# Performance work log

Measured on AMD Instinct MI355X. Metric: run time of the kernel, lower is better.

The kernel has to match this reference:

```python
import jax, jax.numpy as jnp
import numpy as np

ATTEN_DIM = 64

def setup_inputs() -> dict:
    key = jax.random.key(0)
    ks = jax.random.split(key, 7)
    b, c, h, w = 16, 2048, 32, 32
    d_att, d_emb = 64, 64
    x = jax.random.normal(ks[0], (b, c, h, w), dtype=jnp.float32)
    # 1x1 conv == per-position linear; store weights as [out, in]
    scale = 1.0 / np.sqrt(c)
    wq = jax.random.normal(ks[1], (d_att, c), dtype=jnp.float32) * scale
    wk = jax.random.normal(ks[2], (d_att, c), dtype=jnp.float32) * scale
    wv = jax.random.normal(ks[3], (d_emb, c), dtype=jnp.float32) * scale
    bq = jnp.zeros((d_att,), dtype=jnp.float32)
    bk = jnp.zeros((d_att,), dtype=jnp.float32)
    bv = jnp.zeros((d_emb,), dtype=jnp.float32)
    return {"x": x, "wq": wq, "bq": bq, "wk": wk, "bk": bk, "wv": wv, "bv": bv}


def reference(x, wq, bq, wk, bk, wv, bv):
    b, c, h, w = x.shape
    # 1x1 conv projections: [b,c,h,w] x [d,c] -> [b,d,h,w]
    q = jnp.einsum('bchw,dc->bdhw', x, wq) + bq[None, :, None, None]
    k = jnp.einsum('bchw,dc->bdhw', x, wk) + bk[None, :, None, None]
    v = jnp.einsum('bchw,dc->bdhw', x, wv) + bv[None, :, None, None]
    # full non-local attention scores [b, h, w, h, w]
    atten = jnp.einsum('bcxy,bcij->bxyij', q, k) / ATTEN_DIM  # NOTE: module divides by atten_dim, not sqrt
    atten = jax.nn.softmax(atten.reshape(b, h, w, h * w), axis=-1).reshape(b, h, w, h, w)
    out = jnp.einsum('bxyij,bdij->bxyd', atten, v)
    return jnp.transpose(out, (0, 3, 1, 2))  # [b, emb_dim, h, w]
```

## Files before the change

kernel.cpp:

```cpp
#include <hip/hip_runtime.h>

typedef float f32x4 __attribute__((ext_vector_type(4)));
typedef short s16x8 __attribute__((ext_vector_type(8)));
typedef unsigned short u16;
typedef unsigned short u16x8 __attribute__((ext_vector_type(8)));

__device__ __forceinline__ u16 f2bf(float f) {
  unsigned u = __builtin_bit_cast(unsigned, f);
  u += 0x7fffu + ((u >> 16) & 1u);
  return (u16)(u >> 16);
}

__device__ __forceinline__ unsigned cvt_pk_bf16(float a, float b) {
  unsigned r;
  asm("v_cvt_pk_bf16_f32 %0, %1, %2" : "=v"(r) : "v"(a), "v"(b));
  return r;
}

#define AS1 __attribute__((address_space(1)))
#define AS3 __attribute__((address_space(3)))
#define GLD16(g, l) __builtin_amdgcn_global_load_lds((const AS1 unsigned int*)(g), (AS3 unsigned int*)(l), 16, 0, 0)

__global__ __launch_bounds__(256) void prepack_w(
    const float* __restrict__ wq, const float* __restrict__ wk, const float* __restrict__ wv,
    u16* __restrict__ Wpk)
{
  const int d = blockIdx.x;
  const int t = threadIdx.x;
  const int kc = t >> 3, blk = t & 7;
  const int key = (d >> 1) & 7;
  const float* src = (d < 64) ? (wq + (size_t)d * 2048)
                   : (d < 128) ? (wk + (size_t)(d - 64) * 2048)
                               : (wv + (size_t)(d - 128) * 2048);
  const float* s8 = src + kc * 64 + ((blk ^ key) << 3);
  u16x8 o;
#pragma unroll
  for (int j = 0; j < 8; ++j) o[j] = f2bf(s8[j]);
  *(u16x8*)(Wpk + ((size_t)(kc * 192 + d) << 6) + (blk << 3)) = o;
}

__global__ __launch_bounds__(512) void qkv_proj(
    const float* __restrict__ x, const u16* __restrict__ Wpk,
    const float* __restrict__ bq, const float* __restrict__ bk, const float* __restrict__ bv,
    u16* __restrict__ Qo, u16* __restrict__ Ko, u16* __restrict__ Vt)
{
  const int b   = blockIdx.x >> 4;
  const int p0  = (blockIdx.x & 15) * 64;
  const int tid = threadIdx.x;
  const int lane = tid & 63;
  const int wid  = tid >> 6;
  const int l15 = lane & 15, l4 = lane >> 4;
  const int wm = wid & 1, wn = wid >> 1;

  __shared__ __align__(16) u16 lA[4][64 * 64];
  __shared__ __align__(16) u16 lB[4][192 * 64];

  const int pg = lane & 15;
  const int kb = wid * 4 + (lane >> 4);
  const int k0 = kb * 4;
  const int ww = wid - 4;

  f32x4 acc[2][3];
#pragma unroll
  for (int m = 0; m < 2; ++m)
#pragma unroll
    for (int n = 0; n < 3; ++n) acc[m][n] = (f32x4)(0.0f);

  const float* xb = x + (size_t)b * 2048 * 1024 + p0 + pg * 4;

  float4 SA[8], SB[8];

  auto xload2 = [&](int c, float4 (&S)[8]) {
#pragma unroll
    for (int cc = 0; cc < 2; ++cc) {
      const float* g = xb + (size_t)((c + cc) * 64 + k0) * 1024;
#pragma unroll
      for (int r = 0; r < 4; ++r) S[cc * 4 + r] = *(const float4*)(g + r * 1024);
    }
  };
  auto xstore2 = [&](int c, float4 (&S)[8]) {
#pragma unroll
    for (int cc = 0; cc < 2; ++cc) {
      const int slot = (c + cc) & 3;
#pragma unroll
      for (int col = 0; col < 4; ++col) {
        int p = pg * 4 + col;
        unsigned lo = cvt_pk_bf16(S[cc * 4 + 0][col], S[cc * 4 + 1][col]);
        unsigned hi = cvt_pk_bf16(S[cc * 4 + 2][col], S[cc * 4 + 3][col]);
        int swz = ((kb >> 1) ^ ((p >> 1) & 7)) & 7;
        char* dst = (char*)&lA[0][0] + slot * 8192 + p * 128 + (swz << 4) + (kb & 1) * 8;
        *(uint2*)dst = make_uint2(lo, hi);
      }
    }
  };
  auto wissue2 = [&](int c) {
#pragma unroll
    for (int cc = 0; cc < 2; ++cc) {
      const int slot = (c + cc) & 3;
      const u16* g = Wpk + (size_t)(c + cc) * 12288 + lane * 8;
#pragma unroll
      for (int j = 0; j < 6; ++j) {
        int q = ww * 6 + j;
        GLD16(g + q * 512, &lB[0][0] + slot * 12288 + q * 512);
      }
    }
  };
  auto domfma = [&](int slot) {
#pragma unroll
    for (int ks = 0; ks < 2; ++ks) {
      s16x8 af[2], bfv[3];
#pragma unroll
      for (int m = 0; m < 2; ++m) {
        int p = wm * 32 + m * 16 + l15;
        int swz = ((ks * 4 + l4) ^ ((p >> 1) & 7)) & 7;
        af[m] = *(const s16x8*)((const char*)&lA[0][0] + slot * 8192 + p * 128 + (swz << 4));
      }
#pragma unroll
      for (int n = 0; n < 3; ++n) {
        int d = wn * 48 + n * 16 + l15;
        int swz = ((ks * 4 + l4) ^ ((d >> 1) & 7)) & 7;
        bfv[n] = *(const s16x8*)((const char*)&lB[0][0] + slot * 24576 + d * 128 + (swz << 4));
      }
#pragma unroll
      for (int m = 0; m < 2; ++m)
#pragma unroll
        for (int n = 0; n < 3; ++n)
          acc[m][n] = __builtin_amdgcn_mfma_f32_16x16x32_bf16(af[m], bfv[n], acc[m][n], 0, 0, 0);
    }
  };
  auto barrier = [&]() {
    if (wid < 4) asm volatile("s_waitcnt lgkmcnt(0)" ::: "memory");
    else         asm volatile("s_waitcnt vmcnt(0) lgkmcnt(0)" ::: "memory");
    __builtin_amdgcn_sched_barrier(0);
    __builtin_amdgcn_s_barrier();
    __builtin_amdgcn_sched_barrier(0);
  };
  auto step = [&](int t, float4 (&Sl)[8], float4 (&Ss)[8]) {
    if (wid < 4) { if (t < 14) xload2(2 * t + 4, Sl); }
    else         { if (t < 15) wissue2(2 * t + 2); }
    __builtin_amdgcn_s_setprio(1);
    domfma((2 * t) & 3);
    domfma((2 * t + 1) & 3);
    __builtin_amdgcn_s_setprio(0);
    if (wid < 4 && t < 15) xstore2(2 * t + 2, Ss);
    barrier();
  };

  if (wid < 4) { xload2(0, SA); xload2(2, SB); xstore2(0, SA); }
  else         { wissue2(0); }
  barrier();

  for (int tt = 0; tt < 8; ++tt) {
    step(2 * tt,     SA, SB);
    step(2 * tt + 1, SB, SA);
  }

#pragma unroll
  for (int n = 0; n < 3; ++n) {
    const int dg = wn * 48 + n * 16 + l15;
    const int wi = dg >> 6, dl = dg & 63;
    const float* bsrc = (wi == 0) ? bq : (wi == 1) ? bk : bv;
    const float bias = bsrc[dl];
#pragma unroll
    for (int m = 0; m < 2; ++m) {
      const int pl = wm * 32 + m * 16 + l4 * 4;
      f32x4 a = acc[m][n];
      if (wi < 2) {
        u16* dst = (wi == 0 ? Qo : Ko) + ((size_t)b * 1024 + p0 + pl) * 64 + dl;
#pragma unroll
        for (int r = 0; r < 4; ++r) dst[(size_t)r * 64] = f2bf(a[r] + bias);
      } else {
        ushort4 hh;
        hh.x = f2bf(a[0] + bias); hh.y = f2bf(a[1] + bias);
        hh.z = f2bf(a[2] + bias); hh.w = f2bf(a[3] + bias);
        *(ushort4*)(Vt + ((size_t)b * 64 + dl) * 1024 + p0 + pl) = hh;
      }
    }
  }
}

__global__ __launch_bounds__(256) void attn_kernel(
    const u16* __restrict__ Qg, const u16* __restrict__ Kg,
    const u16* __restrict__ Vg, float* __restrict__ Po, float* __restrict__ lp)
{
  const int bid = blockIdx.x;
  const int b  = bid >> 5;
  const int qt = (bid >> 1) & 15;
  const int h  = bid & 1;
  const int q0 = qt * 64;
  const int tid = threadIdx.x;
  const int lane = tid & 63;
  const int wid = tid >> 6;
  const int l15 = lane & 15, l4 = lane >> 4;
  const int qb = q0 + wid * 16;

  __shared__ __align__(16) u16 lK[2][128 * 64];
  __shared__ __align__(16) u16 lV[2][64 * 128];
  __shared__ __align__(16) u16 lP[4][16 * 128];

  s16x8 qa[2];
#pragma unroll
  for (int ks = 0; ks < 2; ++ks)
    qa[ks] = *(const s16x8*)(Qg + ((size_t)b * 1024 + qb + l15) * 64 + ks * 32 + l4 * 8);

  float l_run[4];
  f32x4 oacc[4];
#pragma unroll
  for (int r = 0; r < 4; ++r) l_run[r] = 0.f;
#pragma unroll
  for (int n = 0; n < 4; ++n) oacc[n] = (f32x4)(0.0f);

  u16x8 kp[4], vp[4];
  auto load_kv = [&](int kc) {
    const int pk0 = kc * 128;
#pragma unroll
    for (int i = 0; i < 4; ++i) {
      int idx = tid + 256 * i;
      int row = idx >> 3, blk = idx & 7;
      kp[i] = *(const u16x8*)(Kg + ((size_t)b * 1024 + pk0 + row) * 64 + blk * 8);
      int vr = idx >> 4, vbk = idx & 15;
      vp[i] = *(const u16x8*)(Vg + ((size_t)b * 64 + vr) * 1024 + pk0 + vbk * 8);
    }
  };
  auto store_kv = [&](int buf) {
#pragma unroll
    for (int i = 0; i < 4; ++i) {
      int idx = tid + 256 * i;
      int row = idx >> 3, blk = idx & 7;
      *(u16x8*)(&lK[buf][0] + row * 64 + ((blk ^ ((row >> 1) & 7)) << 3)) = kp[i];
      int vr = idx >> 4, vbk = idx & 15;
      *(u16x8*)(&lV[buf][0] + vr * 128 + ((vbk ^ ((vr & 7) << 1)) << 3)) = vp[i];
    }
  };

  const int kc0 = h * 4;
  load_kv(kc0); store_kv(0); __syncthreads();

  const float CEXP = 0.0225422933f;

  for (int ic = 0; ic < 4; ++ic) {
    const int cur = ic & 1;
    if (ic + 1 < 4) load_kv(kc0 + ic + 1);

    f32x4 sacc[8];
#pragma unroll
    for (int n = 0; n < 8; ++n) sacc[n] = (f32x4)(0.0f);
#pragma unroll
    for (int ks = 0; ks < 2; ++ks) {
#pragma unroll
      for (int n = 0; n < 8; ++n) {
        int row = n * 16 + l15;
        s16x8 kv = *(const s16x8*)(&lK[cur][0] + row * 64 +
                     (((ks * 4 + l4) ^ ((row >> 1) & 7)) << 3));
        sacc[n] = __builtin_amdgcn_mfma_f32_16x16x32_bf16(qa[ks], kv, sacc[n], 0, 0, 0);
      }
    }

#pragma unroll
    for (int r = 0; r < 4; ++r) {
      const int prow = l4 * 4 + r;
      float psum = 0.f;
#pragma unroll
      for (int n = 0; n < 8; ++n) {
        float pv = exp2f(sacc[n][r] * CEXP);
        psum += pv;
        int blk = (n * 2 + (l15 >> 3)) ^ ((prow & 7) << 1);
        lP[wid][prow * 128 + blk * 8 + (l15 & 7)] = f2bf(pv);
      }
      psum += __shfl_xor(psum, 1);
      psum += __shfl_xor(psum, 2);
      psum += __shfl_xor(psum, 4);
      psum += __shfl_xor(psum, 8);
      l_run[r] += psum;
    }

#pragma unroll
    for (int ks = 0; ks < 4; ++ks) {
      s16x8 pfr = *(const s16x8*)(&lP[wid][0] + l15 * 128 +
                    (((ks * 4 + l4) ^ ((l15 & 7) << 1)) << 3));
#pragma unroll
      for (int n = 0; n < 4; ++n) {
        int row = n * 16 + l15;
        s16x8 vv = *(const s16x8*)(&lV[cur][0] + row * 128 +
                     (((ks * 4 + l4) ^ ((row & 7) << 1)) << 3));
        oacc[n] = __builtin_amdgcn_mfma_f32_16x16x32_bf16(pfr, vv, oacc[n], 0, 0, 0);
      }
    }

    if (ic + 1 < 4) store_kv(cur ^ 1);
    __syncthreads();
  }

#pragma unroll
  for (int n = 0; n < 4; ++n) {
    const int d = n * 16 + l15;
    float4 o;
    o.x = oacc[n][0]; o.y = oacc[n][1]; o.z = oacc[n][2]; o.w = oacc[n][3];
    *(float4*)(Po + (((size_t)h * 16 + b) * 64 + d) * 1024 + q0 + wid * 16 + l4 * 4) = o;
  }
  if (l15 == 0) {
#pragma unroll
    for (int r = 0; r < 4; ++r)
      lp[((size_t)h * 16 + b) * 1024 + qb + l4 * 4 + r] = l_run[r];
  }
}

__global__ __launch_bounds__(256) void attn_merge(
    const float* __restrict__ Po, const float* __restrict__ lp, float* __restrict__ out)
{
  const int i = (blockIdx.x * 256 + threadIdx.x) * 4;
  float4 a = *(const float4*)(Po + i);
  float4 c = *(const float4*)(Po + 1048576 + i);
  const int b = i >> 16;
  const int p = i & 1023;
  const float* l0 = lp + b * 1024 + p;
  const float* l1 = lp + 16384 + b * 1024 + p;
  float4 o;
  o.x = (a.x + c.x) / (l0[0] + l1[0]);
  o.y = (a.y + c.y) / (l0[1] + l1[1]);
  o.z = (a.z + c.z) / (l0[2] + l1[2]);
  o.w = (a.w + c.w) / (l0[3] + l1[3]);
  *(float4*)(out + i) = o;
}

extern "C" void kernel_launch(void* const* d_in, const int* in_sizes, int n_in,
                              void* d_out, int out_size, void* d_ws, size_t ws_size,
                              hipStream_t stream) {
  const float* x  = (const float*)d_in[0];
  const float* wq = (const float*)d_in[1];
  const float* bq = (const float*)d_in[2];
  const float* wk = (const float*)d_in[3];
  const float* bk = (const float*)d_in[4];
  const float* wv = (const float*)d_in[5];
  const float* bv = (const float*)d_in[6];
  float* out = (float*)d_out;

  u16* Qo  = (u16*)d_ws;
  u16* Ko  = Qo + (size_t)16 * 1024 * 64;
  u16* Vt  = Ko + (size_t)16 * 1024 * 64;
  u16* Wpk = Vt + (size_t)16 * 1024 * 64;
  float* Po = (float*)(Wpk + (size_t)32 * 192 * 64);
  float* lpart = Po + (size_t)2 * 16 * 64 * 1024;

  prepack_w<<<192, 256, 0, stream>>>(wq, wk, wv, Wpk);
  qkv_proj<<<256, 512, 0, stream>>>(x, Wpk, bq, bk, bv, Qo, Ko, Vt);
  attn_kernel<<<512, 256, 0, stream>>>(Qo, Ko, Vt, Po, lpart);
  attn_merge<<<1024, 256, 0, stream>>>(Po, lpart, out);
}
```

Baseline: 58.76 us.

## Restructure QKV projection into split-K wave groups with all-wave loading

The QKV projection kernel drops the producer/consumer wave split, where four waves loaded x and four loaded W. All eight waves now share the x and W loads with double-buffered LDS, and the two wave groups alternate on K-chunks. Each wave computes a full 64x48 tile, and the two groups' partial accumulators are reduced through LDS at the end. This aims to spread load latency across all waves and overlap it with MFMA, at the cost of a barrier every chunk, an extra LDS reduction, and more accumulator registers per wave.

```diff
diff --git a/kernel.cpp b/kernel.cpp
--- a/kernel.cpp
+++ b/kernel.cpp
@@ -50,130 +50,138 @@
   const int lane = tid & 63;
   const int wid  = tid >> 6;
   const int l15 = lane & 15, l4 = lane >> 4;
-  const int wm = wid & 1, wn = wid >> 1;
-
-  __shared__ __align__(16) u16 lA[4][64 * 64];
-  __shared__ __align__(16) u16 lB[4][192 * 64];
-
-  const int pg = lane & 15;
-  const int kb = wid * 4 + (lane >> 4);
-  const int k0 = kb * 4;
-  const int ww = wid - 4;
-
-  f32x4 acc[2][3];
-#pragma unroll
-  for (int m = 0; m < 2; ++m)
+  const int cw  = wid & 3;
+  const int grp = wid >> 2;
+
+  __shared__ __align__(16) char smem[65536];
+
+  const int kbq = wid * 2 + (l4 >> 1);
+  const int rp  = (l4 & 1) * 2;
+  const int pc0 = l15 * 4;
+
+  f32x4 acc[4][3];
+#pragma unroll
+  for (int m = 0; m < 4; ++m)
 #pragma unroll
     for (int n = 0; n < 3; ++n) acc[m][n] = (f32x4)(0.0f);
 
-  const float* xb = x + (size_t)b * 2048 * 1024 + p0 + pg * 4;
-
-  float4 SA[8], SB[8];
-
-  auto xload2 = [&](int c, float4 (&S)[8]) {
-#pragma unroll
-    for (int cc = 0; cc < 2; ++cc) {
-      const float* g = xb + (size_t)((c + cc) * 64 + k0) * 1024;
-#pragma unroll
-      for (int r = 0; r < 4; ++r) S[cc * 4 + r] = *(const float4*)(g + r * 1024);
-    }
-  };
-  auto xstore2 = [&](int c, float4 (&S)[8]) {
-#pragma unroll
-    for (int cc = 0; cc < 2; ++cc) {
-      const int slot = (c + cc) & 3;
-#pragma unroll
-      for (int col = 0; col < 4; ++col) {
-        int p = pg * 4 + col;
-        unsigned lo = cvt_pk_bf16(S[cc * 4 + 0][col], S[cc * 4 + 1][col]);
-        unsigned hi = cvt_pk_bf16(S[cc * 4 + 2][col], S[cc * 4 + 3][col]);
-        int swz = ((kb >> 1) ^ ((p >> 1) & 7)) & 7;
-        char* dst = (char*)&lA[0][0] + slot * 8192 + p * 128 + (swz << 4) + (kb & 1) * 8;
-        *(uint2*)dst = make_uint2(lo, hi);
-      }
-    }
-  };
-  auto wissue2 = [&](int c) {
-#pragma unroll
-    for (int cc = 0; cc < 2; ++cc) {
-      const int slot = (c + cc) & 3;
-      const u16* g = Wpk + (size_t)(c + cc) * 12288 + lane * 8;
-#pragma unroll
-      for (int j = 0; j < 6; ++j) {
-        int q = ww * 6 + j;
-        GLD16(g + q * 512, &lB[0][0] + slot * 12288 + q * 512);
-      }
+  const float* xb = x + (size_t)b * 2048 * 1024 + p0 + pc0;
+  float4 xr[2][2];
+
+  auto xissue = [&](int c, int buf) {
+    const float* g = xb + (size_t)(c * 64 + kbq * 4 + rp) * 1024;
+    xr[buf][0] = *(const float4*)g;
+    xr[buf][1] = *(const float4*)(g + 1024);
+  };
+  auto xwrite = [&](int c, int buf) {
+    char* base = smem + (c & 1) * 8192;
+#pragma unroll
+    for (int col = 0; col < 4; ++col) {
+      int p = pc0 + col;
+      unsigned pk = cvt_pk_bf16(xr[buf][0][col], xr[buf][1][col]);
+      char* dst = base + p * 128 + (((kbq >> 1) ^ ((p >> 1) & 7)) << 4)
+                + (kbq & 1) * 8 + (rp >> 1) * 4;
+      *(unsigned*)dst = pk;
+    }
+  };
+  auto wissue = [&](int c) {
+    const u16* g = Wpk + (size_t)c * 12288 + lane * 8;
+    char* base = smem + 16384 + (c & 1) * 24576;
+#pragma unroll
+    for (int j = 0; j < 3; ++j) {
+      int q = wid * 3 + j;
+      GLD16(g + q * 512, base + q * 1024);
     }
   };
   auto domfma = [&](int slot) {
+    const char* aB = smem + slot * 8192;
+    const char* bB = smem + 16384 + slot * 24576;
 #pragma unroll
     for (int ks = 0; ks < 2; ++ks) {
-      s16x8 af[2], bfv[3];
-#pragma unroll
-      for (int m = 0; m < 2; ++m) {
-        int p = wm * 32 + m * 16 + l15;
+      s16x8 af[4], bfv[3];
+#pragma unroll
+      for (int m = 0; m < 4; ++m) {
+        int p = m * 16 + l15;
         int swz = ((ks * 4 + l4) ^ ((p >> 1) & 7)) & 7;
-        af[m] = *(const s16x8*)((const char*)&lA[0][0] + slot * 8192 + p * 128 + (swz << 4));
+        af[m] = *(const s16x8*)(aB + p * 128 + (swz << 4));
       }
 #pragma unroll
       for (int n = 0; n < 3; ++n) {
-        int d = wn * 48 + n * 16 + l15;
+        int d = cw * 48 + n * 16 + l15;
         int swz = ((ks * 4 + l4) ^ ((d >> 1) & 7)) & 7;
-        bfv[n] = *(const s16x8*)((const char*)&lB[0][0] + slot * 24576 + d * 128 + (swz << 4));
-      }
-#pragma unroll
-      for (int m = 0; m < 2; ++m)
+        bfv[n] = *(const s16x8*)(bB + d * 128 + (swz << 4));
+      }
+#pragma unroll
+      for (int m = 0; m < 4; ++m)
 #pragma unroll
         for (int n = 0; n < 3; ++n)
           acc[m][n] = __builtin_amdgcn_mfma_f32_16x16x32_bf16(af[m], bfv[n], acc[m][n], 0, 0, 0);
     }
   };
-  auto barrier = [&]() {
-    if (wid < 4) asm volatile("s_waitcnt lgkmcnt(0)" ::: "memory");
-    else         asm volatile("s_waitcnt vmcnt(0) lgkmcnt(0)" ::: "memory");
+
+  wissue(0);
+  xissue(0, 0);
+  xissue(1, 1);
+  asm volatile("s_waitcnt vmcnt(2)" ::: "memory");
+  __builtin_amdgcn_sched_barrier(0);
+  xwrite(0, 0);
+  asm volatile("s_waitcnt lgkmcnt(0)" ::: "memory");
+  __builtin_amdgcn_sched_barrier(0);
+  __builtin_amdgcn_s_barrier();
+  __builtin_amdgcn_sched_barrier(0);
+
+  for (int c = 0; c < 32; ++c) {
+    if (c < 31) wissue(c + 1);
+    if (c < 30) xissue(c + 2, c & 1);
+    if (grp == (c & 1)) {
+      __builtin_amdgcn_s_setprio(1);
+      domfma(c & 1);
+      __builtin_amdgcn_s_setprio(0);
+    }
+    if (c < 31) xwrite(c + 1, (c + 1) & 1);
+    if (c < 30) asm volatile("s_waitcnt vmcnt(2) lgkmcnt(0)" ::: "memory");
+    else        asm volatile("s_waitcnt vmcnt(0) lgkmcnt(0)" ::: "memory");
     __builtin_amdgcn_sched_barrier(0);
     __builtin_amdgcn_s_barrier();
     __builtin_amdgcn_sched_barrier(0);
-  };
-  auto step = [&](int t, float4 (&Sl)[8], float4 (&Ss)[8]) {
-    if (wid < 4) { if (t < 14) xload2(2 * t + 4, Sl); }
-    else         { if (t < 15) wissue2(2 * t + 2); }
-    __builtin_amdgcn_s_setprio(1);
-    domfma((2 * t) & 3);
-    domfma((2 * t + 1) & 3);
-    __builtin_amdgcn_s_setprio(0);
-    if (wid < 4 && t < 15) xstore2(2 * t + 2, Ss);
-    barrier();
-  };
-
-  if (wid < 4) { xload2(0, SA); xload2(2, SB); xstore2(0, SA); }
-  else         { wissue2(0); }
-  barrier();
-
-  for (int tt = 0; tt < 8; ++tt) {
-    step(2 * tt,     SA, SB);
-    step(2 * tt + 1, SB, SA);
-  }
-
-#pragma unroll
-  for (int n = 0; n < 3; ++n) {
-    const int dg = wn * 48 + n * 16 + l15;
-    const int wi = dg >> 6, dl = dg & 63;
-    const float* bsrc = (wi == 0) ? bq : (wi == 1) ? bk : bv;
-    const float bias = bsrc[dl];
-#pragma unroll
-    for (int m = 0; m < 2; ++m) {
-      const int pl = wm * 32 + m * 16 + l4 * 4;
-      f32x4 a = acc[m][n];
-      if (wi < 2) {
-        u16* dst = (wi == 0 ? Qo : Ko) + ((size_t)b * 1024 + p0 + pl) * 64 + dl;
-#pragma unroll
-        for (int r = 0; r < 4; ++r) dst[(size_t)r * 64] = f2bf(a[r] + bias);
-      } else {
-        ushort4 hh;
-        hh.x = f2bf(a[0] + bias); hh.y = f2bf(a[1] + bias);
-        hh.z = f2bf(a[2] + bias); hh.w = f2bf(a[3] + bias);
-        *(ushort4*)(Vt + ((size_t)b * 64 + dl) * 1024 + p0 + pl) = hh;
+  }
+
+  if (grp == 1) {
+#pragma unroll
+    for (int m = 0; m < 4; ++m)
+#pragma unroll
+      for (int n = 0; n < 3; ++n)
+        *(f32x4*)(smem + cw * 12288 + ((m * 3 + n) * 64 + lane) * 16) = acc[m][n];
+  }
+  asm volatile("s_waitcnt lgkmcnt(0)" ::: "memory");
+  __builtin_amdgcn_s_barrier();
+  if (grp == 0) {
+#pragma unroll
+    for (int m = 0; m < 4; ++m)
+#pragma unroll
+      for (int n = 0; n < 3; ++n)
+        acc[m][n] += *(const f32x4*)(smem + cw * 12288 + ((m * 3 + n) * 64 + lane) * 16);
+
+#pragma unroll
+    for (int n = 0; n < 3; ++n) {
+      const int dg = cw * 48 + n * 16 + l15;
+      const int wi = dg >> 6, dl = dg & 63;
+      const float* bsrc = (wi == 0) ? bq : (wi == 1) ? bk : bv;
+      const float bias = bsrc[dl];
+#pragma unroll
+      for (int m = 0; m < 4; ++m) {
+        const int pl = m * 16 + l4 * 4;
+        f32x4 a = acc[m][n];
+        if (wi < 2) {
+          u16* dst = (wi == 0 ? Qo : Ko) + ((size_t)b * 1024 + p0 + pl) * 64 + dl;
+#pragma unroll
+          for (int r = 0; r < 4; ++r) dst[(size_t)r * 64] = f2bf(a[r] + bias);
+        } else {
+          ushort4 hh;
+          hh.x = f2bf(a[0] + bias); hh.y = f2bf(a[1] + bias);
+          hh.z = f2bf(a[2] + bias); hh.w = f2bf(a[3] + bias);
+          *(ushort4*)(Vt + ((size_t)b * 64 + dl) * 1024 + p0 + pl) = hh;
+        }
       }
     }
   }
```

Measured after the change: 80.43 us. 1.37x slower.

## Pre-swizzle K/V in projection and stream tiles via direct global-to-LDS loads

Applied to the files above, without the earlier changes.

The projection epilogue now folds the softmax exponent scale into Q and writes K and V already in the swizzled LDS layout. This lets the attention kernel use global_load_lds DMA to fill double-buffered K/V tiles with vmcnt-based waits instead of register staging. It also raises wave priority around the MFMA phases and packs P to bf16 in pairs. This removes register round-trips and the per-element scale multiply. The cost is tighter coupling between the producer's stored layout and the consumer's swizzle.

```diff
diff --git a/kernel.cpp b/kernel.cpp
--- a/kernel.cpp
+++ b/kernel.cpp
@@ -20,6 +20,8 @@
 #define AS1 __attribute__((address_space(1)))
 #define AS3 __attribute__((address_space(3)))
 #define GLD16(g, l) __builtin_amdgcn_global_load_lds((const AS1 unsigned int*)(g), (AS3 unsigned int*)(l), 16, 0, 0)
+
+#define CEXP 0.0225421101f
 
 __global__ __launch_bounds__(256) void prepack_w(
     const float* __restrict__ wq, const float* __restrict__ wk, const float* __restrict__ wv,
@@ -67,7 +69,6 @@
     for (int n = 0; n < 3; ++n) acc[m][n] = (f32x4)(0.0f);
 
   const float* xb = x + (size_t)b * 2048 * 1024 + p0 + pg * 4;
-
   float4 SA[8], SB[8];
 
   auto xload2 = [&](int c, float4 (&S)[8]) {
@@ -165,15 +166,25 @@
     for (int m = 0; m < 2; ++m) {
       const int pl = wm * 32 + m * 16 + l4 * 4;
       f32x4 a = acc[m][n];
-      if (wi < 2) {
-        u16* dst = (wi == 0 ? Qo : Ko) + ((size_t)b * 1024 + p0 + pl) * 64 + dl;
-#pragma unroll
-        for (int r = 0; r < 4; ++r) dst[(size_t)r * 64] = f2bf(a[r] + bias);
+      if (wi == 0) {
+        u16* dst = Qo + ((size_t)b * 1024 + p0 + pl) * 64 + dl;
+#pragma unroll
+        for (int r = 0; r < 4; ++r) dst[(size_t)r * 64] = f2bf((a[r] + bias) * CEXP);
+      } else if (wi == 1) {
+#pragma unroll
+        for (int r = 0; r < 4; ++r) {
+          const int p = p0 + pl + r;
+          Ko[((size_t)b * 1024 + p) * 64 + (((dl >> 3) ^ ((p >> 1) & 7)) << 3) + (dl & 7)]
+            = f2bf(a[r] + bias);
+        }
       } else {
+        const int pk0 = p0 + pl;
         ushort4 hh;
         hh.x = f2bf(a[0] + bias); hh.y = f2bf(a[1] + bias);
         hh.z = f2bf(a[2] + bias); hh.w = f2bf(a[3] + bias);
-        *(ushort4*)(Vt + ((size_t)b * 64 + dl) * 1024 + p0 + pl) = hh;
+        u16* dst = Vt + ((size_t)b * 64 + dl) * 1024 + (pk0 & ~127)
+                 + (((((pk0 >> 3) & 15) ^ ((dl & 7) << 1)) & 15) << 3) + (pk0 & 7);
+        *(ushort4*)dst = hh;
       }
     }
   }
@@ -190,9 +201,9 @@
   const int q0 = qt * 64;
   const int tid = threadIdx.x;
   const int lane = tid & 63;
-  const int wid = tid >> 6;
+  const int w = tid >> 6;
   const int l15 = lane & 15, l4 = lane >> 4;
-  const int qb = q0 + wid * 16;
+  const int qb = q0 + w * 16;
 
   __shared__ __align__(16) u16 lK[2][128 * 64];
   __shared__ __align__(16) u16 lV[2][64 * 128];
@@ -203,6 +214,9 @@
   for (int ks = 0; ks < 2; ++ks)
     qa[ks] = *(const s16x8*)(Qg + ((size_t)b * 1024 + qb + l15) * 64 + ks * 32 + l4 * 8);
 
+  const u16* Kb = Kg + (size_t)b * 65536;
+  const u16* Vb = Vg + (size_t)b * 65536;
+
   float l_run[4];
   f32x4 oacc[4];
 #pragma unroll
@@ -210,62 +224,50 @@
 #pragma unroll
   for (int n = 0; n < 4; ++n) oacc[n] = (f32x4)(0.0f);
 
-  u16x8 kp[4], vp[4];
-  auto load_kv = [&](int kc) {
-    const int pk0 = kc * 128;
-#pragma unroll
-    for (int i = 0; i < 4; ++i) {
-      int idx = tid + 256 * i;
-      int row = idx >> 3, blk = idx & 7;
-      kp[i] = *(const u16x8*)(Kg + ((size_t)b * 1024 + pk0 + row) * 64 + blk * 8);
-      int vr = idx >> 4, vbk = idx & 15;
-      vp[i] = *(const u16x8*)(Vg + ((size_t)b * 64 + vr) * 1024 + pk0 + vbk * 8);
-    }
-  };
-  auto store_kv = [&](int buf) {
-#pragma unroll
-    for (int i = 0; i < 4; ++i) {
-      int idx = tid + 256 * i;
-      int row = idx >> 3, blk = idx & 7;
-      *(u16x8*)(&lK[buf][0] + row * 64 + ((blk ^ ((row >> 1) & 7)) << 3)) = kp[i];
-      int vr = idx >> 4, vbk = idx & 15;
-      *(u16x8*)(&lV[buf][0] + vr * 128 + ((vbk ^ ((vr & 7) << 1)) << 3)) = vp[i];
-    }
-  };
-
-  const int kc0 = h * 4;
-  load_kv(kc0); store_kv(0); __syncthreads();
-
-  const float CEXP = 0.0225422933f;
-
-  for (int ic = 0; ic < 4; ++ic) {
-    const int cur = ic & 1;
-    if (ic + 1 < 4) load_kv(kc0 + ic + 1);
-
+  auto kv_issue = [&](int tile, int buf) {
+    const int pk0 = tile * 128;
+#pragma unroll
+    for (int jj = 0; jj < 4; ++jj)
+      GLD16(Kb + (size_t)(pk0 + w * 32 + jj * 8) * 64 + lane * 8,
+            (char*)&lK[buf][0] + (w * 4 + jj) * 1024);
+#pragma unroll
+    for (int jj = 0; jj < 4; ++jj)
+      GLD16(Vb + (size_t)(w * 16 + jj * 4 + (lane >> 4)) * 1024 + pk0 + (lane & 15) * 8,
+            (char*)&lV[buf][0] + (w * 4 + jj) * 1024);
+  };
+
+  auto compute = [&](int buf) {
     f32x4 sacc[8];
 #pragma unroll
     for (int n = 0; n < 8; ++n) sacc[n] = (f32x4)(0.0f);
+    __builtin_amdgcn_s_setprio(1);
 #pragma unroll
     for (int ks = 0; ks < 2; ++ks) {
 #pragma unroll
       for (int n = 0; n < 8; ++n) {
         int row = n * 16 + l15;
-        s16x8 kv = *(const s16x8*)(&lK[cur][0] + row * 64 +
+        s16x8 kv = *(const s16x8*)(&lK[buf][0] + row * 64 +
                      (((ks * 4 + l4) ^ ((row >> 1) & 7)) << 3));
         sacc[n] = __builtin_amdgcn_mfma_f32_16x16x32_bf16(qa[ks], kv, sacc[n], 0, 0, 0);
       }
     }
+    __builtin_amdgcn_s_setprio(0);
 
 #pragma unroll
     for (int r = 0; r < 4; ++r) {
       const int prow = l4 * 4 + r;
+      const int key = (prow & 7) << 1;
+      float pv[8];
       float psum = 0.f;
 #pragma unroll
-      for (int n = 0; n < 8; ++n) {
-        float pv = exp2f(sacc[n][r] * CEXP);
-        psum += pv;
-        int blk = (n * 2 + (l15 >> 3)) ^ ((prow & 7) << 1);
-        lP[wid][prow * 128 + blk * 8 + (l15 & 7)] = f2bf(pv);
+      for (int n = 0; n < 8; ++n) { pv[n] = exp2f(sacc[n][r]); psum += pv[n]; }
+#pragma unroll
+      for (int n = 0; n < 8; n += 2) {
+        unsigned pk = cvt_pk_bf16(pv[n], pv[n + 1]);
+        int blk0 = (n * 2 + (l15 >> 3)) ^ key;
+        int blk1 = ((n + 1) * 2 + (l15 >> 3)) ^ key;
+        lP[w][prow * 128 + blk0 * 8 + (l15 & 7)] = (u16)pk;
+        lP[w][prow * 128 + blk1 * 8 + (l15 & 7)] = (u16)(pk >> 16);
       }
       psum += __shfl_xor(psum, 1);
       psum += __shfl_xor(psum, 2);
@@ -274,21 +276,46 @@
       l_run[r] += psum;
     }
 
+    __builtin_amdgcn_s_setprio(1);
 #pragma unroll
     for (int ks = 0; ks < 4; ++ks) {
-      s16x8 pfr = *(const s16x8*)(&lP[wid][0] + l15 * 128 +
+      s16x8 pfr = *(const s16x8*)(&lP[w][0] + l15 * 128 +
                     (((ks * 4 + l4) ^ ((l15 & 7) << 1)) << 3));
 #pragma unroll
       for (int n = 0; n < 4; ++n) {
         int row = n * 16 + l15;
-        s16x8 vv = *(const s16x8*)(&lV[cur][0] + row * 128 +
+        s16x8 vv = *(const s16x8*)(&lV[buf][0] + row * 128 +
                      (((ks * 4 + l4) ^ ((row & 7) << 1)) << 3));
         oacc[n] = __builtin_amdgcn_mfma_f32_16x16x32_bf16(pfr, vv, oacc[n], 0, 0, 0);
       }
     }
-
-    if (ic + 1 < 4) store_kv(cur ^ 1);
-    __syncthreads();
+    __builtin_amdgcn_s_setprio(0);
+  };
+
+  const int t0 = h * 4;
+  kv_issue(t0, 0);
+  kv_issue(t0 + 1, 1);
+  asm volatile("s_waitcnt vmcnt(8)" ::: "memory");
+  __builtin_amdgcn_sched_barrier(0);
+  __builtin_amdgcn_s_barrier();
+  __builtin_amdgcn_sched_barrier(0);
+
+  for (int ic = 0; ic < 4; ++ic) {
+    compute(ic & 1);
+    if (ic < 3) {
+      __builtin_amdgcn_sched_barrier(0);
+      __builtin_amdgcn_s_barrier();
+      __builtin_amdgcn_sched_barrier(0);
+      if (ic + 2 < 4) {
+        kv_issue(t0 + ic + 2, ic & 1);
+        asm volatile("s_waitcnt vmcnt(8)" ::: "memory");
+      } else {
+        asm volatile("s_waitcnt vmcnt(0)" ::: "memory");
+      }
+      __builtin_amdgcn_sched_barrier(0);
+      __builtin_amdgcn_s_barrier();
+      __builtin_amdgcn_sched_barrier(0);
+    }
   }
 
 #pragma unroll
@@ -296,7 +323,7 @@
     const int d = n * 16 + l15;
     float4 o;
     o.x = oacc[n][0]; o.y = oacc[n][1]; o.z = oacc[n][2]; o.w = oacc[n][3];
-    *(float4*)(Po + (((size_t)h * 16 + b) * 64 + d) * 1024 + q0 + wid * 16 + l4 * 4) = o;
+    *(float4*)(Po + (((size_t)h * 16 + b) * 64 + d) * 1024 + q0 + w * 16 + l4 * 4) = o;
   }
   if (l15 == 0) {
 #pragma unroll
```

Result: faster. 57.26 us (-2.6%).
